# Optimization experiments

Measured on AMD Instinct MI355X. Metric: run time of the kernel, lower is better.

## Reference

```python
import jax, jax.numpy as jnp
import numpy as np
from jax.scipy.special import logsumexp

OFFSET = 2.0
SIG_OFF = 1.0 - 1.0 / (1.0 + np.exp(-OFFSET))  # 1 - sigmoid(offset)
EPS = 1e-22  # matches Flow++ safe_log clamp


def safe_log(x):
    return jnp.log(jnp.clip(x, EPS))


def setup_inputs() -> dict:
    key = jax.random.key(0)
    ks = jax.random.split(key, 6)
    B, K, C, L = 16, 16, 64, 2048
    x_change = jax.random.normal(ks[0], (B, C, L), jnp.float32)
    a = jax.random.normal(ks[1], (B, C, L), jnp.float32)
    b = jax.random.normal(ks[2], (B, C, L), jnp.float32)
    pi = jax.random.normal(ks[3], (B, K, C, L), jnp.float32)
    mu = jax.random.normal(ks[4], (B, K, C, L), jnp.float32)
    s = jax.random.normal(ks[5], (B, K, C, L), jnp.float32) * 0.1
    sldj = jnp.zeros((B,), jnp.float32)
    return {"x_change": x_change, "a": a, "b": b, "pi": pi, "mu": mu, "s": s, "sldj": sldj}


def reference(x_change, a, b, pi, mu, s, sldj):
    # Mixture-of-logistics coupling, forward direction (reverse=False, use_logmix=True).
    log_pi = jax.nn.log_softmax(pi, axis=1)                 # (B,K,C,L)
    z = (x_change[:, None] - mu) * jnp.exp(-s)              # (B,K,C,L) standardized
    # mixture_log_cdf: logsumexp_k [ log_pi_k + log sigmoid(z_k) ]
    log_cdf = logsumexp(log_pi + jax.nn.log_sigmoid(z), axis=1)   # (B,C,L)
    # mixture_log_pdf: logistic log-pdf = z - log_scale - 2*softplus(z)
    logistic_ldj = logsumexp(log_pi + z - s - 2.0 * jax.nn.softplus(z), axis=1)  # (B,C,L)
    u = jnp.exp(log_cdf)                                    # in (0,1)
    # sigmoid-inverse (logit) + its log-det: -log u - log(1-u)
    out = -safe_log(1.0 / u - 1.0)
    scale_ldj = -safe_log(u) - safe_log(1.0 - u)
    scale = jax.nn.sigmoid(a + OFFSET) + SIG_OFF
    B = x_change.shape[0]
    sldj = sldj + jnp.sum((logistic_ldj + scale_ldj + jnp.log(scale)).reshape(B, -1), axis=-1)
    out = (out + b) * scale
    return out, sldj
```

## Files before the change

kernel.cpp:

```cpp
#include <hip/hip_runtime.h>
#include <math.h>

constexpr int Bn   = 16;
constexpr int Kn   = 16;
constexpr int Cn   = 64;
constexpr int Ln   = 2048;
constexpr int CL   = Cn * Ln;
constexpr int Ntot = Bn * CL;
constexpr int VEC  = 8;
constexpr int TPB  = 256;
constexpr int EPB  = TPB * VEC;
constexpr int NBLK = Ntot / EPB;
constexpr int BLK_PER_B = CL / EPB;

constexpr float SIG_OFF = 0.11920292202211755f;
constexpr float TINY    = 1e-36f;

__global__ __launch_bounds__(TPB) void flowpp_fwd(
    const float* __restrict__ x,  const float* __restrict__ a,
    const float* __restrict__ bb, const float* __restrict__ pi,
    const float* __restrict__ mu, const float* __restrict__ s,
    float* __restrict__ out, float* __restrict__ wsp)
{
    const int tid = threadIdx.x;
    const int e0  = blockIdx.x * EPB + tid * VEC;
    const int b   = blockIdx.x / BLK_PER_B;

    const float4 x40 = *(const float4*)(x  + e0);
    const float4 x41 = *(const float4*)(x  + e0 + 4);
    const float4 a40 = *(const float4*)(a  + e0);
    const float4 a41 = *(const float4*)(a  + e0 + 4);
    const float4 b40 = *(const float4*)(bb + e0);
    const float4 b41 = *(const float4*)(bb + e0 + 4);

    const float xv[VEC] = {x40.x, x40.y, x40.z, x40.w, x41.x, x41.y, x41.z, x41.w};

    float S1[VEC], S2[VEC], S3[VEC], S4[VEC];
    #pragma unroll
    for (int i = 0; i < VEC; ++i) { S1[i] = S2[i] = S3[i] = S4[i] = 0.f; }

    const int kbase = b * (Kn * CL) + (e0 - b * CL);
    const float* __restrict__ pp = pi + kbase;
    const float* __restrict__ mp = mu + kbase;
    const float* __restrict__ sp = s  + kbase;

    #pragma unroll 4
    for (int k = 0; k < Kn; ++k) {
        const int off = k * CL;
        const float4 p40  = *(const float4*)(pp + off);
        const float4 p41  = *(const float4*)(pp + off + 4);
        const float4 m40  = *(const float4*)(mp + off);
        const float4 m41  = *(const float4*)(mp + off + 4);
        const float4 sc40 = *(const float4*)(sp + off);
        const float4 sc41 = *(const float4*)(sp + off + 4);
        const float pk[VEC] = {p40.x, p40.y, p40.z, p40.w, p41.x, p41.y, p41.z, p41.w};
        const float mk[VEC] = {m40.x, m40.y, m40.z, m40.w, m41.x, m41.y, m41.z, m41.w};
        const float sk[VEC] = {sc40.x, sc40.y, sc40.z, sc40.w, sc41.x, sc41.y, sc41.z, sc41.w};
        #pragma unroll
        for (int i = 0; i < VEC; ++i) {
            float es = __expf(-sk[i]);
            float z  = (xv[i] - mk[i]) * es;
            float ez = __expf(-z);
            float g  = __builtin_amdgcn_rcpf(1.f + ez);
            float e1 = __expf(pk[i]);
            float t2 = e1 * g;
            float t4 = t2 * ez;
            float t3 = t4 * g * es;
            S1[i] += e1;
            S2[i] += t2;
            S4[i] += t4;
            S3[i] += t3;
        }
    }

    const float av[VEC] = {a40.x, a40.y, a40.z, a40.w, a41.x, a41.y, a41.z, a41.w};
    const float bv[VEC] = {b40.x, b40.y, b40.z, b40.w, b41.x, b41.y, b41.z, b41.w};

    float contrib = 0.f;
    float outv[VEC];
    #pragma unroll
    for (int i = 0; i < VEC; ++i) {
        float LA = __logf(fmaxf(S1[i], TINY));
        float LB = __logf(fmaxf(S2[i], TINY));
        float LC = __logf(fmaxf(S3[i], TINY));
        float LD = __logf(fmaxf(S4[i], TINY));
        float sc = __builtin_amdgcn_rcpf(1.f + __expf(-(av[i] + 2.f))) + SIG_OFF;
        contrib += LC + LA - LB - LD + __logf(sc);
        outv[i] = (LB - LD + bv[i]) * sc;
    }

    *(float4*)(out + e0)     = make_float4(outv[0], outv[1], outv[2], outv[3]);
    *(float4*)(out + e0 + 4) = make_float4(outv[4], outv[5], outv[6], outv[7]);

    #pragma unroll
    for (int off = 32; off; off >>= 1)
        contrib += __shfl_down(contrib, off);
    __shared__ float red[TPB / 64];
    if ((tid & 63) == 0) red[tid >> 6] = contrib;
    __syncthreads();
    if (tid == 0) {
        float t = red[0];
        #pragma unroll
        for (int wv = 1; wv < TPB / 64; ++wv) t += red[wv];
        wsp[blockIdx.x] = t;
    }
}

__global__ __launch_bounds__(64) void flowpp_sldj_reduce(
    const float* __restrict__ wsp, const float* __restrict__ sldj_in,
    float* __restrict__ sldj_out)
{
    const int b = blockIdx.x;
    const int t = threadIdx.x;
    float v = wsp[b * BLK_PER_B + t];
    #pragma unroll
    for (int off = 32; off; off >>= 1)
        v += __shfl_down(v, off);
    if (t == 0) sldj_out[b] = sldj_in[b] + v;
}

extern "C" void kernel_launch(void* const* d_in, const int* in_sizes, int n_in,
                              void* d_out, int out_size, void* d_ws, size_t ws_size,
                              hipStream_t stream) {
    const float* x    = (const float*)d_in[0];
    const float* a    = (const float*)d_in[1];
    const float* bb   = (const float*)d_in[2];
    const float* pi   = (const float*)d_in[3];
    const float* mu   = (const float*)d_in[4];
    const float* s    = (const float*)d_in[5];
    const float* sldj = (const float*)d_in[6];

    float* out      = (float*)d_out;
    float* sldj_out = (float*)d_out + Ntot;
    float* wsp      = (float*)d_ws;

    flowpp_fwd<<<NBLK, TPB, 0, stream>>>(x, a, bb, pi, mu, s, out, wsp);
    flowpp_sldj_reduce<<<Bn, 64, 0, stream>>>(wsp, sldj, sldj_out);
}
```

Baseline: 86.54 us.

## Prefetch mixture loads, use nontemporal access, fuse sldj reduce via last-block atomics

Raises the block size to 1024 threads and software-pipelines the k-loop so the next component's pi/mu/s vectors load while the current one is computed. Streaming loads and stores use nontemporal hints, and the a/b loads move after the loop to shorten register lifetimes. The separate sldj reduction kernel is replaced by an atomic counter per batch, where the last block sums the partials; a small kernel zeroes the counters first. This trades one launch for another and adds atomics, and the 1024-thread blocks with fewer of them may cut occupancy or load balance.

```diff
diff --git a/kernel.cpp b/kernel.cpp
--- a/kernel.cpp
+++ b/kernel.cpp
@@ -8,7 +8,7 @@
 constexpr int CL   = Cn * Ln;
 constexpr int Ntot = Bn * CL;
 constexpr int VEC  = 8;
-constexpr int TPB  = 256;
+constexpr int TPB  = 1024;
 constexpr int EPB  = TPB * VEC;
 constexpr int NBLK = Ntot / EPB;
 constexpr int BLK_PER_B = CL / EPB;
@@ -16,23 +16,29 @@
 constexpr float SIG_OFF = 0.11920292202211755f;
 constexpr float TINY    = 1e-36f;
 
+typedef float fv4 __attribute__((ext_vector_type(4)));
+
+__global__ __launch_bounds__(64) void zero_counters(unsigned* __restrict__ cnt) {
+    if (threadIdx.x < Bn) cnt[threadIdx.x] = 0u;
+}
+
+__device__ __forceinline__ fv4 ntl4(const float* p) {
+    return __builtin_nontemporal_load((const fv4*)p);
+}
+
 __global__ __launch_bounds__(TPB) void flowpp_fwd(
     const float* __restrict__ x,  const float* __restrict__ a,
     const float* __restrict__ bb, const float* __restrict__ pi,
     const float* __restrict__ mu, const float* __restrict__ s,
-    float* __restrict__ out, float* __restrict__ wsp)
+    const float* __restrict__ sldj_in,
+    float* __restrict__ out, float* __restrict__ wsp, unsigned* __restrict__ cnt)
 {
     const int tid = threadIdx.x;
     const int e0  = blockIdx.x * EPB + tid * VEC;
     const int b   = blockIdx.x / BLK_PER_B;
 
-    const float4 x40 = *(const float4*)(x  + e0);
-    const float4 x41 = *(const float4*)(x  + e0 + 4);
-    const float4 a40 = *(const float4*)(a  + e0);
-    const float4 a41 = *(const float4*)(a  + e0 + 4);
-    const float4 b40 = *(const float4*)(bb + e0);
-    const float4 b41 = *(const float4*)(bb + e0 + 4);
-
+    const fv4 x40 = *(const fv4*)(x + e0);
+    const fv4 x41 = *(const fv4*)(x + e0 + 4);
     const float xv[VEC] = {x40.x, x40.y, x40.z, x40.w, x41.x, x41.y, x41.z, x41.w};
 
     float S1[VEC], S2[VEC], S3[VEC], S4[VEC];
@@ -44,18 +50,23 @@
     const float* __restrict__ mp = mu + kbase;
     const float* __restrict__ sp = s  + kbase;
 
-    #pragma unroll 4
+    fv4 p40 = ntl4(pp),     p41 = ntl4(pp + 4);
+    fv4 m40 = ntl4(mp),     m41 = ntl4(mp + 4);
+    fv4 sc40 = ntl4(sp),    sc41 = ntl4(sp + 4);
+
     for (int k = 0; k < Kn; ++k) {
-        const int off = k * CL;
-        const float4 p40  = *(const float4*)(pp + off);
-        const float4 p41  = *(const float4*)(pp + off + 4);
-        const float4 m40  = *(const float4*)(mp + off);
-        const float4 m41  = *(const float4*)(mp + off + 4);
-        const float4 sc40 = *(const float4*)(sp + off);
-        const float4 sc41 = *(const float4*)(sp + off + 4);
-        const float pk[VEC] = {p40.x, p40.y, p40.z, p40.w, p41.x, p41.y, p41.z, p41.w};
-        const float mk[VEC] = {m40.x, m40.y, m40.z, m40.w, m41.x, m41.y, m41.z, m41.w};
-        const float sk[VEC] = {sc40.x, sc40.y, sc40.z, sc40.w, sc41.x, sc41.y, sc41.z, sc41.w};
+        const fv4 cp0 = p40,  cp1 = p41;
+        const fv4 cm0 = m40,  cm1 = m41;
+        const fv4 cs0 = sc40, cs1 = sc41;
+        if (k + 1 < Kn) {
+            const int off = (k + 1) * CL;
+            p40  = ntl4(pp + off);  p41  = ntl4(pp + off + 4);
+            m40  = ntl4(mp + off);  m41  = ntl4(mp + off + 4);
+            sc40 = ntl4(sp + off);  sc41 = ntl4(sp + off + 4);
+        }
+        const float pk[VEC] = {cp0.x, cp0.y, cp0.z, cp0.w, cp1.x, cp1.y, cp1.z, cp1.w};
+        const float mk[VEC] = {cm0.x, cm0.y, cm0.z, cm0.w, cm1.x, cm1.y, cm1.z, cm1.w};
+        const float sk[VEC] = {cs0.x, cs0.y, cs0.z, cs0.w, cs1.x, cs1.y, cs1.z, cs1.w};
         #pragma unroll
         for (int i = 0; i < VEC; ++i) {
             float es = __expf(-sk[i]);
@@ -73,6 +84,10 @@
         }
     }
 
+    const fv4 a40 = *(const fv4*)(a  + e0);
+    const fv4 a41 = *(const fv4*)(a  + e0 + 4);
+    const fv4 b40 = *(const fv4*)(bb + e0);
+    const fv4 b41 = *(const fv4*)(bb + e0 + 4);
     const float av[VEC] = {a40.x, a40.y, a40.z, a40.w, a41.x, a41.y, a41.z, a41.w};
     const float bv[VEC] = {b40.x, b40.y, b40.z, b40.w, b41.x, b41.y, b41.z, b41.w};
 
@@ -89,34 +104,35 @@
         outv[i] = (LB - LD + bv[i]) * sc;
     }
 
-    *(float4*)(out + e0)     = make_float4(outv[0], outv[1], outv[2], outv[3]);
-    *(float4*)(out + e0 + 4) = make_float4(outv[4], outv[5], outv[6], outv[7]);
+    fv4 o0 = {outv[0], outv[1], outv[2], outv[3]};
+    fv4 o1 = {outv[4], outv[5], outv[6], outv[7]};
+    __builtin_nontemporal_store(o0, (fv4*)(out + e0));
+    __builtin_nontemporal_store(o1, (fv4*)(out + e0 + 4));
 
+    float c = contrib;
     #pragma unroll
-    for (int off = 32; off; off >>= 1)
-        contrib += __shfl_down(contrib, off);
+    for (int off = 32; off; off >>= 1) c += __shfl_down(c, off);
     __shared__ float red[TPB / 64];
-    if ((tid & 63) == 0) red[tid >> 6] = contrib;
+    __shared__ int lastFlag;
+    if ((tid & 63) == 0) red[tid >> 6] = c;
     __syncthreads();
     if (tid == 0) {
         float t = red[0];
         #pragma unroll
         for (int wv = 1; wv < TPB / 64; ++wv) t += red[wv];
-        wsp[blockIdx.x] = t;
+        __hip_atomic_store(&wsp[blockIdx.x], t, __ATOMIC_RELEASE, __HIP_MEMORY_SCOPE_AGENT);
+        unsigned old = __hip_atomic_fetch_add(&cnt[b], 1u, __ATOMIC_ACQ_REL, __HIP_MEMORY_SCOPE_AGENT);
+        lastFlag = (old == (unsigned)(BLK_PER_B - 1));
     }
-}
-
-__global__ __launch_bounds__(64) void flowpp_sldj_reduce(
-    const float* __restrict__ wsp, const float* __restrict__ sldj_in,
-    float* __restrict__ sldj_out)
-{
-    const int b = blockIdx.x;
-    const int t = threadIdx.x;
-    float v = wsp[b * BLK_PER_B + t];
-    #pragma unroll
-    for (int off = 32; off; off >>= 1)
-        v += __shfl_down(v, off);
-    if (t == 0) sldj_out[b] = sldj_in[b] + v;
+    __syncthreads();
+    if (lastFlag && tid < 64) {
+        float v = 0.f;
+        if (tid < BLK_PER_B)
+            v = __hip_atomic_load(&wsp[b * BLK_PER_B + tid], __ATOMIC_RELAXED, __HIP_MEMORY_SCOPE_AGENT);
+        #pragma unroll
+        for (int off = 32; off; off >>= 1) v += __shfl_down(v, off);
+        if (tid == 0) out[Ntot + b] = sldj_in[b] + v;
+    }
 }
 
 extern "C" void kernel_launch(void* const* d_in, const int* in_sizes, int n_in,
@@ -131,9 +147,9 @@
     const float* sldj = (const float*)d_in[6];
 
     float* out      = (float*)d_out;
-    float* sldj_out = (float*)d_out + Ntot;
-    float* wsp      = (float*)d_ws;
+    float*    wsp   = (float*)d_ws;
+    unsigned* cnt   = (unsigned*)((char*)d_ws + 4096);
 
-    flowpp_fwd<<<NBLK, TPB, 0, stream>>>(x, a, bb, pi, mu, s, out, wsp);
-    flowpp_sldj_reduce<<<Bn, 64, 0, stream>>>(wsp, sldj, sldj_out);
+    zero_counters<<<1, 64, 0, stream>>>(cnt);
+    flowpp_fwd<<<NBLK, TPB, 0, stream>>>(x, a, bb, pi, mu, s, sldj, out, wsp, cnt);
 }
```

New measurement: 136.8 us. +58.1%, slower.
